# Kernel tuning notes

Measured on AMD Instinct MI355X. Metric: run time of the kernel, lower is better.

## Reference

```python
import jax, jax.numpy as jnp
import numpy as np

P_IN = 32  # MODEL_CONFIG['p_in']; note: all 32 sample points share the same offsets in the source


def _bilinear_border(feat, sx, sy):
    """Replicates F.grid_sample(mode='bilinear', padding_mode='border', align_corners=False)
    for a single point per (b, n). feat: [B,C,H,W]; sx, sy: [B,N] in pixel coords.
    align_corners=False unnormalization of grid built as 2*s/size - 1 gives px = s - 0.5.
    Returns [B,N,C]."""
    H, W = feat.shape[-2], feat.shape[-1]
    px = jnp.clip(sx - 0.5, 0.0, W - 1.0)  # border padding clamps coords
    py = jnp.clip(sy - 0.5, 0.0, H - 1.0)
    x0 = jnp.floor(px)
    y0 = jnp.floor(py)
    wx = (px - x0)[..., None]  # [B,N,1]
    wy = (py - y0)[..., None]
    x0i = x0.astype(jnp.int32)
    y0i = y0.astype(jnp.int32)
    x1i = jnp.minimum(x0i + 1, W - 1)
    y1i = jnp.minimum(y0i + 1, H - 1)

    def gather(f, yi, xi):  # f [C,H,W], yi/xi [N] -> [N,C]
        return f[:, yi, xi].T

    g = jax.vmap(gather)  # over batch
    v00 = g(feat, y0i, x0i)
    v01 = g(feat, y0i, x1i)
    v10 = g(feat, y1i, x0i)
    v11 = g(feat, y1i, x1i)
    return (v00 * (1 - wx) * (1 - wy) + v01 * wx * (1 - wy)
            + v10 * (1 - wx) * wy + v11 * wx * wy)


def _forward(feats, query_pos, query_content, W_off, b_off, sigma_z):
    offsets = query_content @ W_off + b_off  # [B,N,3]
    x, y, z, r = (query_pos[..., i] for i in range(4))
    dx, dy, dz = offsets[..., 0], offsets[..., 1], offsets[..., 2]
    sx = x + dx * (2.0 ** (z - r))
    sy = y + dy * (2.0 ** (z + r))
    sz = z + dz
    L = len(feats)
    levels = jnp.arange(L, dtype=sz.dtype)
    # gaussian z weight, then softmax over levels (as in source: softmax of the exp values)
    w = jnp.exp(-((sz[..., None] - levels) ** 2) / (2.0 * sigma_z ** 2))  # [B,N,L]
    zw = jax.nn.softmax(w, axis=-1)
    out = sum(zw[..., l:l + 1] * _bilinear_border(feats[l], sx, sy) for l in range(L))  # [B,N,C]
    B, N, C = out.shape
    # all P_IN sample points use identical coords in the source -> broadcast
    return jnp.broadcast_to(out[:, :, None, :], (B, N, P_IN, C))


def setup_inputs() -> dict:
    key = jax.random.key(0)
    ks = jax.random.split(key, 8)
    B, N, C = 8, 300, 256
    sizes = [(100, 100), (50, 50), (25, 25), (13, 13)]
    feats = [jax.random.normal(ks[i], (B, C, h, w), dtype=jnp.float32)
             for i, (h, w) in enumerate(sizes)]
    u = jax.random.uniform(ks[4], (B, N, 4), dtype=jnp.float32)
    # x in [0,100), y in [0,100) (level-0 pixel coords), z in [0,4), r in [0,1)
    query_pos = u * jnp.array([100.0, 100.0, 4.0, 1.0], dtype=jnp.float32)
    query_content = jax.random.normal(ks[5], (B, N, C), dtype=jnp.float32)
    W_off = jax.random.normal(ks[6], (C, 3), dtype=jnp.float32) * 0.02
    b_off = jnp.zeros((3,), dtype=jnp.float32)
    sigma_z = jnp.ones((1,), dtype=jnp.float32) * 0.5
    return {"feat0": feats[0], "feat1": feats[1], "feat2": feats[2], "feat3": feats[3],
            "query_pos": query_pos, "query_content": query_content,
            "W_off": W_off, "b_off": b_off, "sigma_z": sigma_z}


def reference(feat0, feat1, feat2, feat3, query_pos, query_content, W_off, b_off, sigma_z):
    return _forward([feat0, feat1, feat2, feat3], query_pos, query_content, W_off, b_off, sigma_z)
```

## Files before the change

### kernel.cpp

```cpp
#include <hip/hip_runtime.h>

constexpr int Bc = 8;
constexpr int Nc = 300;
constexpr int Cc = 256;
constexpr int Pc = 32;

typedef float f32x4 __attribute__((ext_vector_type(4)));

constexpr int LVL_OFF[4] = {0, 10000, 12500, 13125};
constexpr int SLICE_FLOATS = 13294;

__device__ __forceinline__ void gl_lds16(const void* g, void* l) {
    __builtin_amdgcn_global_load_lds(
        (const __attribute__((address_space(1))) void*)g,
        (__attribute__((address_space(3))) void*)l, 16, 0, 0);
}
__device__ __forceinline__ void gl_lds4(const void* g, void* l) {
    __builtin_amdgcn_global_load_lds(
        (const __attribute__((address_space(1))) void*)g,
        (__attribute__((address_space(3))) void*)l, 4, 0, 0);
}

__global__ __launch_bounds__(256) void params_kernel(
    const float* __restrict__ qpos, const float* __restrict__ qcont,
    const float* __restrict__ Woff, const float* __restrict__ boff,
    const float* __restrict__ sigma, float* __restrict__ params)
{
    const int w = threadIdx.x >> 6;
    const int lane = threadIdx.x & 63;
    const int q = blockIdx.x * 4 + w;

    f32x4 qc = *(const f32x4*)&qcont[(size_t)q * Cc + lane * 4];
    float p0 = 0.f, p1 = 0.f, p2 = 0.f;
#pragma unroll
    for (int j = 0; j < 4; ++j) {
        const float* wr = &Woff[(lane * 4 + j) * 3];
        p0 += qc[j] * wr[0];
        p1 += qc[j] * wr[1];
        p2 += qc[j] * wr[2];
    }
#pragma unroll
    for (int off = 32; off > 0; off >>= 1) {
        p0 += __shfl_down(p0, off, 64);
        p1 += __shfl_down(p1, off, 64);
        p2 += __shfl_down(p2, off, 64);
    }
    if (lane == 0) {
        float dx = p0 + boff[0];
        float dy = p1 + boff[1];
        float dz = p2 + boff[2];
        float x = qpos[q * 4 + 0];
        float y = qpos[q * 4 + 1];
        float z = qpos[q * 4 + 2];
        float r = qpos[q * 4 + 3];
        float sx = x + dx * exp2f(z - r);
        float sy = y + dy * exp2f(z + r);
        float sz = z + dz;
        float sg = sigma[0];
        float inv = 1.0f / (2.0f * sg * sg);
        float e[4];
        float s = 0.f;
#pragma unroll
        for (int l = 0; l < 4; ++l) {
            float d = sz - (float)l;
            float wgt = __expf(-d * d * inv);
            e[l] = __expf(wgt);
            s += e[l];
        }
        float rs = 1.0f / s;
        params[q * 8 + 0] = sx;
        params[q * 8 + 1] = sy;
#pragma unroll
        for (int l = 0; l < 4; ++l) params[q * 8 + 2 + l] = e[l] * rs;
    }
}

__device__ __forceinline__ float lerp_lds(const float* __restrict__ base, int W,
                                          float sx, float sy)
{
    float px = fminf(fmaxf(sx - 0.5f, 0.f), (float)(W - 1));
    float py = fminf(fmaxf(sy - 0.5f, 0.f), (float)(W - 1));
    float x0f = floorf(px);
    float y0f = floorf(py);
    float wx = px - x0f;
    float wy = py - y0f;
    int x0 = (int)x0f;
    int y0 = (int)y0f;
    int x1 = min(x0 + 1, W - 1);
    int y1 = min(y0 + 1, W - 1);
    float v00 = base[y0 * W + x0];
    float v01 = base[y0 * W + x1];
    float v10 = base[y1 * W + x0];
    float v11 = base[y1 * W + x1];
    float top = v00 + wx * (v01 - v00);
    float bot = v10 + wx * (v11 - v10);
    return top + wy * (bot - top);
}

__device__ __forceinline__ void issue_slice_dma(
    const float* __restrict__ f0, const float* __restrict__ f1,
    const float* __restrict__ f2, const float* __restrict__ f3,
    int bc, float* __restrict__ buf, int wave, int lane)
{
    {
        const char* g0 = (const char*)(f0 + (size_t)bc * 10000);
        char* l0 = (char*)&buf[LVL_OFF[0]];
        for (int i = wave; i < 39; i += 4)
            gl_lds16(g0 + i * 1024 + lane * 16, l0 + i * 1024);
        if (wave == 3 && lane < 4)
            gl_lds16(g0 + 39 * 1024 + lane * 16, l0 + 39 * 1024);
    }
    {
        const char* g1 = (const char*)(f1 + (size_t)bc * 2500);
        char* l1 = (char*)&buf[LVL_OFF[1]];
        for (int i = wave; i < 9; i += 4)
            gl_lds16(g1 + i * 1024 + lane * 16, l1 + i * 1024);
        if (wave == 2 && lane < 49)
            gl_lds16(g1 + 9 * 1024 + lane * 16, l1 + 9 * 1024);
    }
    {
        const char* g2 = (const char*)(f2 + (size_t)bc * 625);
        char* l2 = (char*)&buf[LVL_OFF[2]];
        for (int i = wave; i < 9; i += 4)
            gl_lds4(g2 + i * 256 + lane * 4, l2 + i * 256);
        if (wave == 1 && lane < 49)
            gl_lds4(g2 + 9 * 256 + lane * 4, l2 + 9 * 256);
    }
    {
        const char* g3 = (const char*)(f3 + (size_t)bc * 169);
        char* l3 = (char*)&buf[LVL_OFF[3]];
        for (int i = wave; i < 2; i += 4)
            gl_lds4(g3 + i * 256 + lane * 4, l3 + i * 256);
        if (wave == 3 && lane < 41)
            gl_lds4(g3 + 2 * 256 + lane * 4, l3 + 2 * 256);
    }
}

__global__ __launch_bounds__(256) void sample_kernel(
    const float* __restrict__ f0, const float* __restrict__ f1,
    const float* __restrict__ f2, const float* __restrict__ f3,
    const float* __restrict__ params, float* __restrict__ outT)
{
    __shared__ float sl[2][SLICE_FLOATS];
    const int t = threadIdx.x;
    const int wave = t >> 6;
    const int lane = t & 63;
    const int bc0 = blockIdx.x * 4;
    const int b = bc0 >> 8;

    const int q0 = b * Nc + t;
    const bool has2 = (t < Nc - 256);
    const int q1 = q0 + 256;
    float sx0 = params[q0 * 8 + 0];
    float sy0 = params[q0 * 8 + 1];
    float zw0_0 = params[q0 * 8 + 2], zw0_1 = params[q0 * 8 + 3];
    float zw0_2 = params[q0 * 8 + 4], zw0_3 = params[q0 * 8 + 5];
    float sx1 = 0.f, sy1 = 0.f, zw1_0 = 0.f, zw1_1 = 0.f, zw1_2 = 0.f, zw1_3 = 0.f;
    if (has2) {
        sx1 = params[q1 * 8 + 0];
        sy1 = params[q1 * 8 + 1];
        zw1_0 = params[q1 * 8 + 2]; zw1_1 = params[q1 * 8 + 3];
        zw1_2 = params[q1 * 8 + 4]; zw1_3 = params[q1 * 8 + 5];
    }

    issue_slice_dma(f0, f1, f2, f3, bc0, sl[0], wave, lane);
#pragma unroll
    for (int k = 0; k < 4; ++k) {
        __syncthreads();
        if (k + 1 < 4)
            issue_slice_dma(f0, f1, f2, f3, bc0 + k + 1, sl[(k + 1) & 1], wave, lane);

        const float* buf = sl[k & 1];
        const int bc = bc0 + k;
        {
            float acc = zw0_0 * lerp_lds(&buf[LVL_OFF[0]], 100, sx0, sy0)
                      + zw0_1 * lerp_lds(&buf[LVL_OFF[1]],  50, sx0, sy0)
                      + zw0_2 * lerp_lds(&buf[LVL_OFF[2]],  25, sx0, sy0)
                      + zw0_3 * lerp_lds(&buf[LVL_OFF[3]],  13, sx0, sy0);
            outT[(size_t)bc * Nc + t] = acc;
        }
        if (has2) {
            float acc = zw1_0 * lerp_lds(&buf[LVL_OFF[0]], 100, sx1, sy1)
                      + zw1_1 * lerp_lds(&buf[LVL_OFF[1]],  50, sx1, sy1)
                      + zw1_2 * lerp_lds(&buf[LVL_OFF[2]],  25, sx1, sy1)
                      + zw1_3 * lerp_lds(&buf[LVL_OFF[3]],  13, sx1, sy1);
            outT[(size_t)bc * Nc + t + 256] = acc;
        }
    }
}

__global__ __launch_bounds__(256) void broadcast_kernel(
    const float* __restrict__ outT, float* __restrict__ out)
{
    __shared__ float sval[Cc];
    const int q = blockIdx.x;
    const int b = q / Nc;
    const int n = q - b * Nc;
    const int c = threadIdx.x;
    sval[c] = outT[((size_t)(b * Cc + c)) * Nc + n];
    __syncthreads();

    const int wave = threadIdx.x >> 6;
    const int c4 = (threadIdx.x & 63) * 4;
    f32x4 val = *(const f32x4*)&sval[c4];
    float* obase = out + (size_t)q * (Pc * Cc) + c4;
#pragma unroll
    for (int p = wave; p < Pc; p += 4) {
        __builtin_nontemporal_store(val, (f32x4*)(obase + p * Cc));
    }
}

__global__ __launch_bounds__(256) void sampling3d_fallback(
    const float* __restrict__ f0, const float* __restrict__ f1,
    const float* __restrict__ f2, const float* __restrict__ f3,
    const float* __restrict__ qpos, const float* __restrict__ qcont,
    const float* __restrict__ Woff, const float* __restrict__ boff,
    const float* __restrict__ sigma, float* __restrict__ out)
{
    const int q = blockIdx.x;
    const int b = q / Nc;
    const int c = threadIdx.x;
    float qc = qcont[q * Cc + c];
    float p0 = qc * Woff[c * 3 + 0];
    float p1 = qc * Woff[c * 3 + 1];
    float p2 = qc * Woff[c * 3 + 2];
#pragma unroll
    for (int off = 32; off > 0; off >>= 1) {
        p0 += __shfl_down(p0, off, 64);
        p1 += __shfl_down(p1, off, 64);
        p2 += __shfl_down(p2, off, 64);
    }
    __shared__ float red[4][3];
    __shared__ float par[8];
    __shared__ float accs[Cc];
    const int wave = threadIdx.x >> 6;
    if ((threadIdx.x & 63) == 0) { red[wave][0] = p0; red[wave][1] = p1; red[wave][2] = p2; }
    __syncthreads();
    if (threadIdx.x == 0) {
        float dx = red[0][0] + red[1][0] + red[2][0] + red[3][0] + boff[0];
        float dy = red[0][1] + red[1][1] + red[2][1] + red[3][1] + boff[1];
        float dz = red[0][2] + red[1][2] + red[2][2] + red[3][2] + boff[2];
        float x = qpos[q * 4 + 0], y = qpos[q * 4 + 1];
        float z = qpos[q * 4 + 2], r = qpos[q * 4 + 3];
        float sx = x + dx * exp2f(z - r);
        float sy = y + dy * exp2f(z + r);
        float sz = z + dz;
        float sg = sigma[0];
        float inv = 1.0f / (2.0f * sg * sg);
        float e[4]; float s = 0.f;
#pragma unroll
        for (int l = 0; l < 4; ++l) {
            float d = sz - (float)l;
            float w = __expf(-d * d * inv);
            e[l] = __expf(w);
            s += e[l];
        }
        float rs = 1.0f / s;
        par[0] = sx; par[1] = sy;
#pragma unroll
        for (int l = 0; l < 4; ++l) par[2 + l] = e[l] * rs;
    }
    __syncthreads();
    const float sx = par[0];
    const float sy = par[1];
    const float* const fs[4] = {f0, f1, f2, f3};
    const int HWs[4] = {100, 50, 25, 13};
    float acc = 0.f;
#pragma unroll
    for (int l = 0; l < 4; ++l) {
        const int W = HWs[l];
        float px = fminf(fmaxf(sx - 0.5f, 0.f), (float)(W - 1));
        float py = fminf(fmaxf(sy - 0.5f, 0.f), (float)(W - 1));
        float x0f = floorf(px), y0f = floorf(py);
        float wx = px - x0f, wy = py - y0f;
        int x0 = (int)x0f, y0 = (int)y0f;
        int x1 = min(x0 + 1, W - 1), y1 = min(y0 + 1, W - 1);
        const float* base = fs[l] + (size_t)((b * Cc + c) * W) * W;
        float v00 = base[y0 * W + x0];
        float v01 = base[y0 * W + x1];
        float v10 = base[y1 * W + x0];
        float v11 = base[y1 * W + x1];
        float top = v00 + wx * (v01 - v00);
        float bot = v10 + wx * (v11 - v10);
        acc += par[2 + l] * (top + wy * (bot - top));
    }
    accs[c] = acc;
    __syncthreads();
    const int c4 = (threadIdx.x & 63) * 4;
    f32x4 val = *(const f32x4*)&accs[c4];
    float* obase = out + (size_t)q * (Pc * Cc) + c4;
#pragma unroll
    for (int p = wave; p < Pc; p += 4) {
        __builtin_nontemporal_store(val, (f32x4*)(obase + p * Cc));
    }
}

extern "C" void kernel_launch(void* const* d_in, const int* in_sizes, int n_in,
                              void* d_out, int out_size, void* d_ws, size_t ws_size,
                              hipStream_t stream) {
    const float* f0    = (const float*)d_in[0];
    const float* f1    = (const float*)d_in[1];
    const float* f2    = (const float*)d_in[2];
    const float* f3    = (const float*)d_in[3];
    const float* qpos  = (const float*)d_in[4];
    const float* qcont = (const float*)d_in[5];
    const float* Woff  = (const float*)d_in[6];
    const float* boff  = (const float*)d_in[7];
    const float* sigma = (const float*)d_in[8];
    float* out = (float*)d_out;

    const size_t params_bytes = (size_t)Bc * Nc * 8 * sizeof(float);
    const size_t outT_bytes   = (size_t)Bc * Cc * Nc * sizeof(float);

    if (ws_size >= params_bytes + outT_bytes) {
        float* params = (float*)d_ws;
        float* outT   = (float*)((char*)d_ws + params_bytes);
        params_kernel<<<Bc * Nc / 4, 256, 0, stream>>>(qpos, qcont, Woff, boff, sigma, params);
        sample_kernel<<<Bc * Cc / 4, 256, 0, stream>>>(f0, f1, f2, f3, params, outT);
        broadcast_kernel<<<Bc * Nc, 256, 0, stream>>>(outT, out);
    } else {
        sampling3d_fallback<<<Bc * Nc, 256, 0, stream>>>(
            f0, f1, f2, f3, qpos, qcont, Woff, boff, sigma, out);
    }
}
```

Measured before the change: 191.3 us.

## Gather level-0 directly from global, stage only small levels in LDS, one slice per block

The sample kernel no longer copies the whole 100x100 level-0 plane into LDS. It gathers the four level-0 corner values straight from global memory and stages only levels 1-3 (about 13 KB) in LDS. Each block now handles one (batch, channel) slice instead of four, with no double buffering, and declares launch bounds targeting 8 blocks per CU. The aim is to cut LDS traffic and footprint so occupancy and parallelism rise, at the cost of scattered uncoalesced global loads for level 0 and losing the cross-slice prefetch overlap.

```diff
diff --git a/kernel.cpp b/kernel.cpp
--- a/kernel.cpp
+++ b/kernel.cpp
@@ -7,8 +7,10 @@
 
 typedef float f32x4 __attribute__((ext_vector_type(4)));
 
-constexpr int LVL_OFF[4] = {0, 10000, 12500, 13125};
-constexpr int SLICE_FLOATS = 13294;
+constexpr int L1_OFF = 0;
+constexpr int L2_OFF = 2500;
+constexpr int L3_OFF = 3125;
+constexpr int STAGE_FLOATS = 3294;
 
 __device__ __forceinline__ void gl_lds16(const void* g, void* l) {
     __builtin_amdgcn_global_load_lds(
@@ -75,78 +77,41 @@
     }
 }
 
-__device__ __forceinline__ float lerp_lds(const float* __restrict__ base, int W,
-                                          float sx, float sy)
-{
+struct BilinW { int i00, i01, i10, i11; float wx, wy; };
+__device__ __forceinline__ BilinW bilin(int W, float sx, float sy) {
     float px = fminf(fmaxf(sx - 0.5f, 0.f), (float)(W - 1));
     float py = fminf(fmaxf(sy - 0.5f, 0.f), (float)(W - 1));
     float x0f = floorf(px);
     float y0f = floorf(py);
-    float wx = px - x0f;
-    float wy = py - y0f;
     int x0 = (int)x0f;
     int y0 = (int)y0f;
     int x1 = min(x0 + 1, W - 1);
     int y1 = min(y0 + 1, W - 1);
-    float v00 = base[y0 * W + x0];
-    float v01 = base[y0 * W + x1];
-    float v10 = base[y1 * W + x0];
-    float v11 = base[y1 * W + x1];
+    BilinW r;
+    r.wx = px - x0f;
+    r.wy = py - y0f;
+    r.i00 = y0 * W + x0; r.i01 = y0 * W + x1;
+    r.i10 = y1 * W + x0; r.i11 = y1 * W + x1;
+    return r;
+}
+__device__ __forceinline__ float blend(float v00, float v01, float v10, float v11,
+                                       float wx, float wy) {
     float top = v00 + wx * (v01 - v00);
     float bot = v10 + wx * (v11 - v10);
     return top + wy * (bot - top);
 }
 
-__device__ __forceinline__ void issue_slice_dma(
-    const float* __restrict__ f0, const float* __restrict__ f1,
-    const float* __restrict__ f2, const float* __restrict__ f3,
-    int bc, float* __restrict__ buf, int wave, int lane)
-{
-    {
-        const char* g0 = (const char*)(f0 + (size_t)bc * 10000);
-        char* l0 = (char*)&buf[LVL_OFF[0]];
-        for (int i = wave; i < 39; i += 4)
-            gl_lds16(g0 + i * 1024 + lane * 16, l0 + i * 1024);
-        if (wave == 3 && lane < 4)
-            gl_lds16(g0 + 39 * 1024 + lane * 16, l0 + 39 * 1024);
-    }
-    {
-        const char* g1 = (const char*)(f1 + (size_t)bc * 2500);
-        char* l1 = (char*)&buf[LVL_OFF[1]];
-        for (int i = wave; i < 9; i += 4)
-            gl_lds16(g1 + i * 1024 + lane * 16, l1 + i * 1024);
-        if (wave == 2 && lane < 49)
-            gl_lds16(g1 + 9 * 1024 + lane * 16, l1 + 9 * 1024);
-    }
-    {
-        const char* g2 = (const char*)(f2 + (size_t)bc * 625);
-        char* l2 = (char*)&buf[LVL_OFF[2]];
-        for (int i = wave; i < 9; i += 4)
-            gl_lds4(g2 + i * 256 + lane * 4, l2 + i * 256);
-        if (wave == 1 && lane < 49)
-            gl_lds4(g2 + 9 * 256 + lane * 4, l2 + 9 * 256);
-    }
-    {
-        const char* g3 = (const char*)(f3 + (size_t)bc * 169);
-        char* l3 = (char*)&buf[LVL_OFF[3]];
-        for (int i = wave; i < 2; i += 4)
-            gl_lds4(g3 + i * 256 + lane * 4, l3 + i * 256);
-        if (wave == 3 && lane < 41)
-            gl_lds4(g3 + 2 * 256 + lane * 4, l3 + 2 * 256);
-    }
-}
-
-__global__ __launch_bounds__(256) void sample_kernel(
+__global__ __launch_bounds__(256, 8) void sample_kernel(
     const float* __restrict__ f0, const float* __restrict__ f1,
     const float* __restrict__ f2, const float* __restrict__ f3,
     const float* __restrict__ params, float* __restrict__ outT)
 {
-    __shared__ float sl[2][SLICE_FLOATS];
+    __shared__ float sl[STAGE_FLOATS];
+    const int bc = blockIdx.x;
     const int t = threadIdx.x;
+    const int b = bc >> 8;
     const int wave = t >> 6;
     const int lane = t & 63;
-    const int bc0 = blockIdx.x * 4;
-    const int b = bc0 >> 8;
 
     const int q0 = b * Nc + t;
     const bool has2 = (t < Nc - 256);
@@ -163,29 +128,70 @@
         zw1_2 = params[q1 * 8 + 4]; zw1_3 = params[q1 * 8 + 5];
     }
 
-    issue_slice_dma(f0, f1, f2, f3, bc0, sl[0], wave, lane);
-#pragma unroll
-    for (int k = 0; k < 4; ++k) {
-        __syncthreads();
-        if (k + 1 < 4)
-            issue_slice_dma(f0, f1, f2, f3, bc0 + k + 1, sl[(k + 1) & 1], wave, lane);
-
-        const float* buf = sl[k & 1];
-        const int bc = bc0 + k;
-        {
-            float acc = zw0_0 * lerp_lds(&buf[LVL_OFF[0]], 100, sx0, sy0)
-                      + zw0_1 * lerp_lds(&buf[LVL_OFF[1]],  50, sx0, sy0)
-                      + zw0_2 * lerp_lds(&buf[LVL_OFF[2]],  25, sx0, sy0)
-                      + zw0_3 * lerp_lds(&buf[LVL_OFF[3]],  13, sx0, sy0);
-            outT[(size_t)bc * Nc + t] = acc;
-        }
-        if (has2) {
-            float acc = zw1_0 * lerp_lds(&buf[LVL_OFF[0]], 100, sx1, sy1)
-                      + zw1_1 * lerp_lds(&buf[LVL_OFF[1]],  50, sx1, sy1)
-                      + zw1_2 * lerp_lds(&buf[LVL_OFF[2]],  25, sx1, sy1)
-                      + zw1_3 * lerp_lds(&buf[LVL_OFF[3]],  13, sx1, sy1);
-            outT[(size_t)bc * Nc + t + 256] = acc;
-        }
+    {
+        const char* g1 = (const char*)(f1 + (size_t)bc * 2500);
+        char* l1 = (char*)&sl[L1_OFF];
+        for (int i = wave; i < 9; i += 4)
+            gl_lds16(g1 + i * 1024 + lane * 16, l1 + i * 1024);
+        if (wave == 2 && lane < 49)
+            gl_lds16(g1 + 9 * 1024 + lane * 16, l1 + 9 * 1024);
+        const char* g2 = (const char*)(f2 + (size_t)bc * 625);
+        char* l2 = (char*)&sl[L2_OFF];
+        for (int i = wave; i < 9; i += 4)
+            gl_lds4(g2 + i * 256 + lane * 4, l2 + i * 256);
+        if (wave == 1 && lane < 49)
+            gl_lds4(g2 + 9 * 256 + lane * 4, l2 + 9 * 256);
+        const char* g3 = (const char*)(f3 + (size_t)bc * 169);
+        char* l3 = (char*)&sl[L3_OFF];
+        for (int i = wave; i < 2; i += 4)
+            gl_lds4(g3 + i * 256 + lane * 4, l3 + i * 256);
+        if (wave == 3 && lane < 41)
+            gl_lds4(g3 + 2 * 256 + lane * 4, l3 + 2 * 256);
+    }
+
+    const float* base0 = f0 + (size_t)bc * 10000;
+    BilinW w00 = bilin(100, sx0, sy0);
+    float a00 = base0[w00.i00];
+    float a01 = base0[w00.i01];
+    float a10 = base0[w00.i10];
+    float a11 = base0[w00.i11];
+    BilinW w01;
+    float b00 = 0.f, b01 = 0.f, b10 = 0.f, b11 = 0.f;
+    if (has2) {
+        w01 = bilin(100, sx1, sy1);
+        b00 = base0[w01.i00];
+        b01 = base0[w01.i01];
+        b10 = base0[w01.i10];
+        b11 = base0[w01.i11];
+    }
+
+    __syncthreads();
+
+    {
+        BilinW w1 = bilin(50, sx0, sy0);
+        BilinW w2 = bilin(25, sx0, sy0);
+        BilinW w3 = bilin(13, sx0, sy0);
+        float acc = zw0_0 * blend(a00, a01, a10, a11, w00.wx, w00.wy)
+                  + zw0_1 * blend(sl[L1_OFF + w1.i00], sl[L1_OFF + w1.i01],
+                                  sl[L1_OFF + w1.i10], sl[L1_OFF + w1.i11], w1.wx, w1.wy)
+                  + zw0_2 * blend(sl[L2_OFF + w2.i00], sl[L2_OFF + w2.i01],
+                                  sl[L2_OFF + w2.i10], sl[L2_OFF + w2.i11], w2.wx, w2.wy)
+                  + zw0_3 * blend(sl[L3_OFF + w3.i00], sl[L3_OFF + w3.i01],
+                                  sl[L3_OFF + w3.i10], sl[L3_OFF + w3.i11], w3.wx, w3.wy);
+        outT[(size_t)bc * Nc + t] = acc;
+    }
+    if (has2) {
+        BilinW w1 = bilin(50, sx1, sy1);
+        BilinW w2 = bilin(25, sx1, sy1);
+        BilinW w3 = bilin(13, sx1, sy1);
+        float acc = zw1_0 * blend(b00, b01, b10, b11, w01.wx, w01.wy)
+                  + zw1_1 * blend(sl[L1_OFF + w1.i00], sl[L1_OFF + w1.i01],
+                                  sl[L1_OFF + w1.i10], sl[L1_OFF + w1.i11], w1.wx, w1.wy)
+                  + zw1_2 * blend(sl[L2_OFF + w2.i00], sl[L2_OFF + w2.i01],
+                                  sl[L2_OFF + w2.i10], sl[L2_OFF + w2.i11], w2.wx, w2.wy)
+                  + zw1_3 * blend(sl[L3_OFF + w3.i00], sl[L3_OFF + w3.i01],
+                                  sl[L3_OFF + w3.i10], sl[L3_OFF + w3.i11], w3.wx, w3.wy);
+        outT[(size_t)bc * Nc + t + 256] = acc;
     }
 }
 
@@ -316,7 +322,7 @@
         float* params = (float*)d_ws;
         float* outT   = (float*)((char*)d_ws + params_bytes);
         params_kernel<<<Bc * Nc / 4, 256, 0, stream>>>(qpos, qcont, Woff, boff, sigma, params);
-        sample_kernel<<<Bc * Cc / 4, 256, 0, stream>>>(f0, f1, f2, f3, params, outT);
+        sample_kernel<<<Bc * Cc, 256, 0, stream>>>(f0, f1, f2, f3, params, outT);
         broadcast_kernel<<<Bc * Nc, 256, 0, stream>>>(outT, out);
     } else {
         sampling3d_fallback<<<Bc * Nc, 256, 0, stream>>>(
```

Result: no change. 189.6 us (-0.9%).
